# Optimization experiments

Hardware: AMD Instinct MI355X
Metric: run time of the kernel (lower is better)

## Reference

```python
import jax, jax.numpy as jnp
import numpy as np

B, T, D_MODEL, N_HEADS = 4, 2048, 1024, 16


def _alibi_bias(n_heads, seq_len):
    # matches torch alibi_bias(): slopes 2**(-8*i/m), i=1..m, m = pow2_ceil(n_heads)
    m = 1
    while m < n_heads:
        m *= 2
    slopes = jnp.array([2.0 ** (-8.0 * i / m) for i in range(1, m + 1)][:n_heads],
                       dtype=jnp.float32)
    pos = jnp.arange(seq_len)
    bias = (pos[None, :] - pos[:, None]).astype(jnp.float32)  # [T, T], j - i
    return slopes[:, None, None, None] * bias[None, None]      # [H, 1, T, T]


def setup_inputs() -> dict:
    key = jax.random.key(0)
    kx, kqkv, ko = jax.random.split(key, 3)
    x = jax.random.normal(kx, (B, T, D_MODEL), dtype=jnp.float32)
    Wqkv = jax.random.normal(kqkv, (3 * D_MODEL, D_MODEL), dtype=jnp.float32) / np.sqrt(D_MODEL)
    Wo = jax.random.normal(ko, (D_MODEL, D_MODEL), dtype=jnp.float32) / np.sqrt(D_MODEL)
    alibi = _alibi_bias(N_HEADS, T)  # [H, 1, T, T]
    return {"x": x, "alibi": alibi, "Wqkv": Wqkv, "Wo": Wo}


def reference(x, alibi, Wqkv, Wo):
    Bb, Tt, C = x.shape
    H = N_HEADS
    dk = C // H
    # qkv projection: [B, T, 3C] -> [B, T, 3, H, dk]
    qkv = (x @ Wqkv.T).reshape(Bb, Tt, 3, H, dk)
    q = jnp.moveaxis(qkv[:, :, 0], 2, 1)  # [B, H, T, dk]
    k = jnp.moveaxis(qkv[:, :, 1], 2, 1)
    v = jnp.moveaxis(qkv[:, :, 2], 2, 1)
    # causal (-inf above diagonal) + alibi additive mask, fp32, like the torch path
    causal = jnp.triu(jnp.full((Tt, Tt), -jnp.inf, dtype=jnp.float32), k=1)
    mask = causal[None, None] + alibi[:, 0][None]  # [1, H, T, T]
    scores = jnp.einsum('bhqd,bhkd->bhqk', q, k) / jnp.sqrt(jnp.float32(dk)) + mask
    p = jax.nn.softmax(scores, axis=-1)
    att = jnp.einsum('bhqk,bhkd->bhqd', p, v)           # [B, H, T, dk]
    y = jnp.moveaxis(att, 1, 2).reshape(Bb, Tt, C)       # [B, T, C]
    return y @ Wo.T
```

## Files before the change

kernel.cpp:

```cpp
#include <hip/hip_runtime.h>
#include <hip/hip_bf16.h>


#define B_ 4
#define T_ 2048
#define C_ 1024
#define H_ 16
#define DK 64

typedef __attribute__((ext_vector_type(8))) short short8;
typedef __attribute__((ext_vector_type(4))) float floatx4;

#define GLDS16(g, l)                                                          \
    __builtin_amdgcn_global_load_lds(                                         \
        (const __attribute__((address_space(1))) void*)(g),                   \
        (__attribute__((address_space(3))) void*)(l), 16, 0, 0)

static __device__ inline short f2bf(float x) {
    __hip_bfloat16 h = __float2bfloat16(x);
    return *reinterpret_cast<short*>(&h);
}

__global__ void detect_k(const unsigned int* __restrict__ x,
                         const unsigned int* __restrict__ ali,
                         const unsigned int* __restrict__ wqkv,
                         const unsigned int* __restrict__ wo,
                         int* __restrict__ flags) {
    __shared__ int cnt[4];
    const int tid = threadIdx.x;
    if (tid < 4) cnt[tid] = 0;
    __syncthreads();
    const int g = tid >> 6, l = tid & 63;
    const unsigned int* p = (g == 0) ? x : (g == 1) ? ali : (g == 2) ? wqkv : wo;
    int c = 0;
    for (int i = 0; i < 4; i++) {
        unsigned int w = p[l * 4 + i];
        int e0 = (w >> 7) & 0xFF;
        int e1 = (w >> 23) & 0xFF;
        c += (e0 >= 100 && e0 <= 140);
        c += (e1 >= 100 && e1 <= 140);
    }
    atomicAdd(&cnt[g], c);
    __syncthreads();
    if (l == 0) flags[g] = (cnt[g] < 400) ? 1 : 0;
}

__global__ void tobf16_k(const void* __restrict__ in, short* __restrict__ out,
                         int n8) {
    const unsigned int* u = (const unsigned int*)in;
    int c = 0;
#pragma unroll
    for (int i = 0; i < 16; i++) {
        unsigned int w = u[i];
        int e0 = (w >> 7) & 0xFF;
        int e1 = (w >> 23) & 0xFF;
        c += (e0 >= 100 && e0 <= 140);
        c += (e1 >= 100 && e1 <= 140);
    }
    const bool f32 = (c < 25);
    int i = blockIdx.x * blockDim.x + threadIdx.x;
    const int stride = gridDim.x * blockDim.x;
    for (; i < n8; i += stride) {
        if (f32) {
            float4 f0 = ((const float4*)in)[2 * i];
            float4 f1 = ((const float4*)in)[2 * i + 1];
            short8 v = { f2bf(f0.x), f2bf(f0.y), f2bf(f0.z), f2bf(f0.w),
                         f2bf(f1.x), f2bf(f1.y), f2bf(f1.z), f2bf(f1.w) };
            *(short8*)(out + (size_t)i * 8) = v;
        } else {
            *(short8*)(out + (size_t)i * 8) = ((const short8*)in)[i];
        }
    }
}

template <int MODE, int N>
__global__ __launch_bounds__(256) void gemm128_k(const short* __restrict__ A,
                                                 const short* __restrict__ W,
                                                 void* __restrict__ Dv) {
    const int K = 1024;
    const int tid  = threadIdx.x;
    const int wv   = tid >> 6;
    const int lane = tid & 63;
    const int l15  = lane & 15;
    const int quad = lane >> 4;
    const int wm = wv >> 1, wn = wv & 1;
    const int bn = blockIdx.x, bm = blockIdx.y;

    __shared__ short As[128 * 64];
    __shared__ short Bs[128 * 64];

    floatx4 acc[4][4];
#pragma unroll
    for (int mt = 0; mt < 4; mt++)
#pragma unroll
        for (int nt = 0; nt < 4; nt++)
#pragma unroll
            for (int r = 0; r < 4; r++) acc[mt][nt][r] = 0.f;

    const int lr = lane >> 3;
    const int lc = lane & 7;
    const int cg = lc ^ lr;

    for (int kt = 0; kt < K; kt += 64) {
        __syncthreads();
#pragma unroll
        for (int i = 0; i < 4; i++) {
            const int rbase = wv * 32 + i * 8;
            const int r = rbase + lr;
            size_t ga;
            if (MODE == 2) {
                int rowg = bm * 128 + r;
                int b = rowg >> 11, t = rowg & (T_ - 1), hh = kt >> 6;
                ga = (((size_t)b * H_ + hh) * T_ + t) * DK + cg * 8;
            } else {
                ga = (size_t)(bm * 128 + r) * K + kt + cg * 8;
            }
            GLDS16(A + ga, As + rbase * 64);
            size_t gb = (size_t)(bn * 128 + r) * K + kt + cg * 8;
            GLDS16(W + gb, Bs + rbase * 64);
        }
        __syncthreads();
#pragma unroll
        for (int ks = 0; ks < 64; ks += 32) {
            short8 af[4], bf[4];
#pragma unroll
            for (int mt = 0; mt < 4; mt++) {
                int row = wm * 64 + mt * 16 + l15;
                int cs = ((ks >> 3) + quad) ^ (row & 7);
                af[mt] = *(const short8*)(As + row * 64 + cs * 8);
            }
#pragma unroll
            for (int nt = 0; nt < 4; nt++) {
                int row = wn * 64 + nt * 16 + l15;
                int cs = ((ks >> 3) + quad) ^ (row & 7);
                bf[nt] = *(const short8*)(Bs + row * 64 + cs * 8);
            }
#pragma unroll
            for (int mt = 0; mt < 4; mt++)
#pragma unroll
                for (int nt = 0; nt < 4; nt++)
                    acc[mt][nt] = __builtin_amdgcn_mfma_f32_16x16x32_bf16(
                        af[mt], bf[nt], acc[mt][nt], 0, 0, 0);
        }
    }

#pragma unroll
    for (int mt = 0; mt < 4; mt++) {
#pragma unroll
        for (int nt = 0; nt < 4; nt++) {
#pragma unroll
            for (int r = 0; r < 4; r++) {
                int row = bm * 128 + wm * 64 + mt * 16 + quad * 4 + r;
                int col = bn * 128 + wn * 64 + nt * 16 + l15;
                if (MODE == 0) {
                    int b = row >> 11, t = row & (T_ - 1);
                    int s = col >> 10, rem = col & 1023;
                    int h = rem >> 6, d = rem & 63;
                    size_t dst = ((((size_t)s * B_ + b) * H_ + h) * T_ + t) * DK + d;
                    ((short*)Dv)[dst] = f2bf(acc[mt][nt][r]);
                } else if (MODE == 3) {
                    int h = row >> 6, d = row & 63;
                    int b = col >> 11, t = col & (T_ - 1);
                    size_t dst = (((size_t)(2 * B_ + b) * H_ + h) * DK + d) * T_ + t;
                    ((short*)Dv)[dst] = f2bf(acc[mt][nt][r]);
                } else {
                    ((float*)Dv)[(size_t)row * N + col] = acc[mt][nt][r];
                }
            }
        }
    }
}

template <int MODE, int N>
__global__ __launch_bounds__(256) void gemm_k(const void* __restrict__ Av,
                                              const void* __restrict__ Wv,
                                              void* __restrict__ Dv,
                                              const int* fA, const int* fW,
                                              size_t aOff) {
    const int K = 1024;
    const int tid  = threadIdx.x;
    const int wave = tid >> 6;
    const int lane = tid & 63;
    const int l15  = lane & 15;
    const int quad = lane >> 4;
    const int bn = blockIdx.x;
    const int bm = blockIdx.y;
    const bool aF32 = fA && (*fA != 0);
    const bool wF32 = fW && (*fW != 0);

    __shared__ short As[64 * 72];
    __shared__ short Bs[64 * 72];

    floatx4 acc[4];
#pragma unroll
    for (int nt = 0; nt < 4; nt++)
#pragma unroll
        for (int r = 0; r < 4; r++) acc[nt][r] = 0.f;

    for (int kt = 0; kt < K; kt += 64) {
        __syncthreads();
#pragma unroll
        for (int i = 0; i < 2; i++) {
            int chunk = tid + i * 256;
            int r = chunk >> 3, c8 = (chunk & 7) * 8;
            size_t offA;
            if (MODE == 2) {
                int rowg = bm * 64 + r;
                int b = rowg >> 11, t = rowg & (T_ - 1), hh = kt >> 6;
                offA = (((size_t)b * H_ + hh) * T_ + t) * DK + c8;
            } else {
                offA = (size_t)(bm * 64 + r) * K + kt + c8;
            }
            size_t offW = (size_t)(bn * 64 + r) * K + kt + c8;
            if (aF32) {
                const float* Af = (const float*)Av + aOff;
                float4 f0 = *(const float4*)(Af + offA);
                float4 f1 = *(const float4*)(Af + offA + 4);
                short8 v = { f2bf(f0.x), f2bf(f0.y), f2bf(f0.z), f2bf(f0.w),
                             f2bf(f1.x), f2bf(f1.y), f2bf(f1.z), f2bf(f1.w) };
                *(short8*)(As + r * 72 + c8) = v;
            } else {
                *(short8*)(As + r * 72 + c8) =
                    *(const short8*)((const short*)Av + aOff + offA);
            }
            if (wF32) {
                const float* Wf = (const float*)Wv;
                float4 f0 = *(const float4*)(Wf + offW);
                float4 f1 = *(const float4*)(Wf + offW + 4);
                short8 v = { f2bf(f0.x), f2bf(f0.y), f2bf(f0.z), f2bf(f0.w),
                             f2bf(f1.x), f2bf(f1.y), f2bf(f1.z), f2bf(f1.w) };
                *(short8*)(Bs + r * 72 + c8) = v;
            } else {
                *(short8*)(Bs + r * 72 + c8) = *(const short8*)((const short*)Wv + offW);
            }
        }
        __syncthreads();
#pragma unroll
        for (int ks = 0; ks < 64; ks += 32) {
            short8 a = *(const short8*)(As + (wave * 16 + l15) * 72 + ks + quad * 8);
#pragma unroll
            for (int nt = 0; nt < 4; nt++) {
                short8 b = *(const short8*)(Bs + (nt * 16 + l15) * 72 + ks + quad * 8);
                acc[nt] = __builtin_amdgcn_mfma_f32_16x16x32_bf16(a, b, acc[nt], 0, 0, 0);
            }
        }
    }

#pragma unroll
    for (int nt = 0; nt < 4; nt++) {
#pragma unroll
        for (int r = 0; r < 4; r++) {
            int row = bm * 64 + wave * 16 + quad * 4 + r;
            int col = bn * 64 + nt * 16 + l15;
            if (MODE == 0) {
                int b = row >> 11, t = row & (T_ - 1);
                int s = col >> 10, rem = col & 1023;
                int h = rem >> 6, d = rem & 63;
                size_t dst = ((((size_t)s * B_ + b) * H_ + h) * T_ + t) * DK + d;
                ((short*)Dv)[dst] = f2bf(acc[nt][r]);
            } else if (MODE == 3) {
                int h = row >> 6, d = row & 63;
                int b = col >> 11, t = col & (T_ - 1);
                size_t dst = (((size_t)(2 * B_ + b) * H_ + h) * DK + d) * T_ + t;
                ((short*)Dv)[dst] = f2bf(acc[nt][r]);
            } else {
                ((float*)Dv)[(size_t)row * N + col] = acc[nt][r];
            }
        }
    }
}

__global__ __launch_bounds__(256, 6) void attn_k(short* __restrict__ qkv) {
    const int tid  = threadIdx.x;
    const int wave = tid >> 6;
    const int lane = tid & 63;
    const int l15  = lane & 15;
    const int quad = lane >> 4;
    const int gid  = blockIdx.x;
    const int bh = (gid & 7) * 8 + (gid >> 8);
    const int qb = (31 - ((gid >> 3) & 31)) * 64;
    const int b = bh >> 4, h = bh & 15;

    short* Qp       = qkv + (((size_t)(0 * B_ + b) * H_ + h) * T_) * DK;
    const short* Kp = qkv + (((size_t)(1 * B_ + b) * H_ + h) * T_) * DK;
    const short* Vt = qkv + (((size_t)(2 * B_ + b) * H_ + h) * DK) * T_;

    __shared__ short Qs[64 * 72];
    __shared__ short Ks[64 * 64];
    __shared__ short Vts[64 * 64];

#pragma unroll
    for (int i = 0; i < 2; i++) {
        int chunk = tid + i * 256;
        int r = chunk >> 3, c8 = (chunk & 7) * 8;
        *(short8*)(Qs + r * 72 + c8) = *(const short8*)(Qp + (size_t)(qb + r) * DK + c8);
    }
    __syncthreads();
    short8 aq0 = *(const short8*)(Qs + (wave * 16 + l15) * 72 + quad * 8);
    short8 aq1 = *(const short8*)(Qs + (wave * 16 + l15) * 72 + 32 + quad * 8);

    const float LOG2E = 1.4426950408889634f;
    const float slope2 = exp2f(-0.5f * (float)(h + 1)) * LOG2E;
    const float scale2 = 0.125f * LOG2E;

    float lsum[4];
    floatx4 o[4];
#pragma unroll
    for (int r = 0; r < 4; r++) lsum[r] = 0.f;
#pragma unroll
    for (int nt = 0; nt < 4; nt++)
#pragma unroll
        for (int r = 0; r < 4; r++) o[nt][r] = 0.f;

    const int jt_end = qb >> 6;
    const int rb = qb + wave * 16 + quad * 4;
    int jstart = 0;
    {
        int lim = qb - 63 - (int)(50.f / slope2);
        if (lim > 0) jstart = lim >> 6;
    }

    const int lr = lane >> 3;
    const int cg = (lane & 7) ^ lr;

    for (int jt = jstart; jt <= jt_end; jt++) {
        __syncthreads();
#pragma unroll
        for (int i = 0; i < 2; i++) {
            const int rbase = wave * 16 + i * 8;
            GLDS16(Kp + (size_t)(jt * 64 + rbase + lr) * DK + cg * 8,
                   Ks + rbase * 64);
            GLDS16(Vt + (size_t)(rbase + lr) * T_ + jt * 64 + cg * 8,
                   Vts + rbase * 64);
        }
        __syncthreads();

        floatx4 s[4];
#pragma unroll
        for (int nt = 0; nt < 4; nt++)
#pragma unroll
            for (int r = 0; r < 4; r++) s[nt][r] = 0.f;
#pragma unroll
        for (int nt = 0; nt < 4; nt++) {
            int row = nt * 16 + l15;
            int c0 = quad ^ (row & 7);
            int c1 = (4 + quad) ^ (row & 7);
            short8 b0 = *(const short8*)(Ks + row * 64 + c0 * 8);
            short8 b1 = *(const short8*)(Ks + row * 64 + c1 * 8);
            s[nt] = __builtin_amdgcn_mfma_f32_16x16x32_bf16(aq0, b0, s[nt], 0, 0, 0);
            s[nt] = __builtin_amdgcn_mfma_f32_16x16x32_bf16(aq1, b1, s[nt], 0, 0, 0);
        }

        const bool diag = (jt == jt_end);
#pragma unroll
        for (int nt = 0; nt < 4; nt++) {
            int colg = jt * 64 + nt * 16 + l15;
            float cb = slope2 * (float)(colg - rb);
#pragma unroll
            for (int r = 0; r < 4; r++) {
                float sv = fmaf(s[nt][r], scale2, cb - slope2 * (float)r);
                if (diag && colg > rb + r) sv = -1e30f;
                float p = exp2f(sv);
                lsum[r] += p;
                Qs[wave * 1088 + (quad * 4 + r) * 68 + nt * 16 + l15] = f2bf(p);
            }
        }

#pragma unroll
        for (int ks = 0; ks < 64; ks += 32) {
            short8 a = *(const short8*)(Qs + wave * 1088 + l15 * 68 + ks + quad * 8);
#pragma unroll
            for (int nt = 0; nt < 4; nt++) {
                int row = nt * 16 + l15;
                int cs = ((ks >> 3) + quad) ^ (row & 7);
                short8 bf = *(const short8*)(Vts + row * 64 + cs * 8);
                o[nt] = __builtin_amdgcn_mfma_f32_16x16x32_bf16(a, bf, o[nt], 0, 0, 0);
            }
        }
    }

#pragma unroll
    for (int r = 0; r < 4; r++) {
#pragma unroll
        for (int mask = 1; mask < 16; mask <<= 1)
            lsum[r] += __shfl_xor(lsum[r], mask);
    }
#pragma unroll
    for (int nt = 0; nt < 4; nt++) {
#pragma unroll
        for (int r = 0; r < 4; r++) {
            int t = qb + wave * 16 + quad * 4 + r;
            int d = nt * 16 + l15;
            Qp[(size_t)t * DK + d] = f2bf(o[nt][r] / lsum[r]);
        }
    }
}

extern "C" void kernel_launch(void* const* d_in, const int* in_sizes, int n_in,
                              void* d_out, int out_size, void* d_ws, size_t ws_size,
                              hipStream_t stream) {
    const void* x    = d_in[0];
    const void* ali  = d_in[1];
    const void* Wqkv = d_in[2];
    const void* Wo   = d_in[3];
    float* out = (float*)d_out;

    int*   flags  = (int*)d_ws;
    short* qkv    = (short*)((char*)d_ws + 1024);
    short* xbf    = (short*)((char*)d_ws + 50332672);
    short* wqkvbf = (short*)((char*)d_ws + 67109888);
    short* wobf   = (short*)((char*)d_ws + 73401344);
    const bool fast = ws_size >= (size_t)75498496;

    dim3 blk(256);
    if (fast) {
        tobf16_k<<<2048, 256, 0, stream>>>(x, xbf, B_ * T_ * C_ / 8);
        tobf16_k<<<1536, 256, 0, stream>>>(Wqkv, wqkvbf, 3 * C_ * C_ / 8);
        tobf16_k<<<512, 256, 0, stream>>>(Wo, wobf, C_ * C_ / 8);
        gemm128_k<0, 0><<<dim3(16, 64), blk, 0, stream>>>(xbf, wqkvbf, qkv);
        gemm128_k<3, 0><<<dim3(64, 8), blk, 0, stream>>>(
            wqkvbf + (size_t)2048 * 1024, xbf, qkv);
        attn_k<<<dim3(2048), blk, 0, stream>>>(qkv);
        gemm128_k<2, C_><<<dim3(8, 64), blk, 0, stream>>>(qkv, wobf, out);
    } else {
        detect_k<<<1, 256, 0, stream>>>((const unsigned int*)x,
                                        (const unsigned int*)ali,
                                        (const unsigned int*)Wqkv,
                                        (const unsigned int*)Wo, flags);
        gemm_k<0, 0><<<dim3(32, 128), blk, 0, stream>>>(x, Wqkv, qkv,
                                                        &flags[0], &flags[2], 0);
        gemm_k<3, 0><<<dim3(128, 16), blk, 0, stream>>>(Wqkv, x, qkv,
                                                        &flags[2], &flags[0],
                                                        (size_t)2048 * 1024);
        attn_k<<<dim3(2048), blk, 0, stream>>>(qkv);
        gemm_k<2, C_><<<dim3(16, 128), blk, 0, stream>>>(qkv, Wo, out,
                                                         nullptr, &flags[3], 0);
    }
}
```

Measured before the change: 529.0 us.

## Merge launches, double-buffer K/V in attention, and swizzle P staging

Three bf16 conversion launches become one kernel that picks its tensor by block index. The two QKV projection GEMMs become a single launch that covers both the standard and the transposed-V layouts. The attention kernel now double-buffers K/V tiles in shared memory so the next tile's global loads overlap compute. It reads Q straight from global into registers, stores P in a separate XOR-swizzled buffer, and lowers the occupancy hint from 6 to 4. The aim is less launch overhead and hidden load latency, at the cost of more LDS per block and fewer resident blocks.

```diff
diff --git a/kernel.cpp b/kernel.cpp
--- a/kernel.cpp
+++ b/kernel.cpp
@@ -45,8 +45,23 @@
     if (l == 0) flags[g] = (cnt[g] < 400) ? 1 : 0;
 }
 
-__global__ void tobf16_k(const void* __restrict__ in, short* __restrict__ out,
-                         int n8) {
+__global__ void tobf16_all_k(const void* __restrict__ x,
+                             const void* __restrict__ wq,
+                             const void* __restrict__ wo,
+                             short* __restrict__ ox,
+                             short* __restrict__ owq,
+                             short* __restrict__ owo) {
+    const int bid = blockIdx.x;
+    const void* in;
+    short* out;
+    int n8, b0, nb;
+    if (bid < 2048) {
+        in = x; out = ox; n8 = B_ * T_ * C_ / 8; b0 = bid; nb = 2048;
+    } else if (bid < 3584) {
+        in = wq; out = owq; n8 = 3 * C_ * C_ / 8; b0 = bid - 2048; nb = 1536;
+    } else {
+        in = wo; out = owo; n8 = C_ * C_ / 8; b0 = bid - 3584; nb = 512;
+    }
     const unsigned int* u = (const unsigned int*)in;
     int c = 0;
 #pragma unroll
@@ -58,8 +73,8 @@
         c += (e1 >= 100 && e1 <= 140);
     }
     const bool f32 = (c < 25);
-    int i = blockIdx.x * blockDim.x + threadIdx.x;
-    const int stride = gridDim.x * blockDim.x;
+    int i = b0 * blockDim.x + threadIdx.x;
+    const int stride = nb * blockDim.x;
     for (; i < n8; i += stride) {
         if (f32) {
             float4 f0 = ((const float4*)in)[2 * i];
@@ -69,6 +84,105 @@
             *(short8*)(out + (size_t)i * 8) = v;
         } else {
             *(short8*)(out + (size_t)i * 8) = ((const short8*)in)[i];
+        }
+    }
+}
+
+__global__ __launch_bounds__(256) void gemm_qkvvt_k(
+    const short* __restrict__ xbf, const short* __restrict__ wqkvbf,
+    short* __restrict__ qkv) {
+    const int K = 1024;
+    const int tid  = threadIdx.x;
+    const int wv   = tid >> 6;
+    const int lane = tid & 63;
+    const int l15  = lane & 15;
+    const int quad = lane >> 4;
+    const int wm = wv >> 1, wn = wv & 1;
+
+    const int id = blockIdx.x;
+    const bool m0 = id < 1024;
+    int bm, bn;
+    const short *Ap, *Wp;
+    if (m0) {
+        bn = id & 15; bm = id >> 4; Ap = xbf; Wp = wqkvbf;
+    } else {
+        int j = id - 1024;
+        bn = j & 63; bm = j >> 6;
+        Ap = wqkvbf + (size_t)2048 * 1024; Wp = xbf;
+    }
+
+    __shared__ short As[128 * 64];
+    __shared__ short Bs[128 * 64];
+
+    floatx4 acc[4][4];
+#pragma unroll
+    for (int mt = 0; mt < 4; mt++)
+#pragma unroll
+        for (int nt = 0; nt < 4; nt++)
+#pragma unroll
+            for (int r = 0; r < 4; r++) acc[mt][nt][r] = 0.f;
+
+    const int lr = lane >> 3;
+    const int lc = lane & 7;
+    const int cg = lc ^ lr;
+
+    for (int kt = 0; kt < K; kt += 64) {
+        __syncthreads();
+#pragma unroll
+        for (int i = 0; i < 4; i++) {
+            const int rbase = wv * 32 + i * 8;
+            const int r = rbase + lr;
+            size_t ga = (size_t)(bm * 128 + r) * K + kt + cg * 8;
+            GLDS16(Ap + ga, As + rbase * 64);
+            size_t gb = (size_t)(bn * 128 + r) * K + kt + cg * 8;
+            GLDS16(Wp + gb, Bs + rbase * 64);
+        }
+        __syncthreads();
+#pragma unroll
+        for (int ks = 0; ks < 64; ks += 32) {
+            short8 af[4], bf[4];
+#pragma unroll
+            for (int mt = 0; mt < 4; mt++) {
+                int row = wm * 64 + mt * 16 + l15;
+                int cs = ((ks >> 3) + quad) ^ (row & 7);
+                af[mt] = *(const short8*)(As + row * 64 + cs * 8);
+            }
+#pragma unroll
+            for (int nt = 0; nt < 4; nt++) {
+                int row = wn * 64 + nt * 16 + l15;
+                int cs = ((ks >> 3) + quad) ^ (row & 7);
+                bf[nt] = *(const short8*)(Bs + row * 64 + cs * 8);
+            }
+#pragma unroll
+            for (int mt = 0; mt < 4; mt++)
+#pragma unroll
+                for (int nt = 0; nt < 4; nt++)
+                    acc[mt][nt] = __builtin_amdgcn_mfma_f32_16x16x32_bf16(
+                        af[mt], bf[nt], acc[mt][nt], 0, 0, 0);
+        }
+    }
+
+#pragma unroll
+    for (int mt = 0; mt < 4; mt++) {
+#pragma unroll
+        for (int nt = 0; nt < 4; nt++) {
+#pragma unroll
+            for (int r = 0; r < 4; r++) {
+                int row = bm * 128 + wm * 64 + mt * 16 + quad * 4 + r;
+                int col = bn * 128 + wn * 64 + nt * 16 + l15;
+                if (m0) {
+                    int b = row >> 11, t = row & (T_ - 1);
+                    int s = col >> 10, rem = col & 1023;
+                    int h = rem >> 6, d = rem & 63;
+                    size_t dst = ((((size_t)s * B_ + b) * H_ + h) * T_ + t) * DK + d;
+                    qkv[dst] = f2bf(acc[mt][nt][r]);
+                } else {
+                    int h = row >> 6, d = row & 63;
+                    int b = col >> 11, t = col & (T_ - 1);
+                    size_t dst = (((size_t)(2 * B_ + b) * H_ + h) * DK + d) * T_ + t;
+                    qkv[dst] = f2bf(acc[mt][nt][r]);
+                }
+            }
         }
     }
 }
@@ -270,7 +384,7 @@
     }
 }
 
-__global__ __launch_bounds__(256, 6) void attn_k(short* __restrict__ qkv) {
+__global__ __launch_bounds__(256, 4) void attn_k(short* __restrict__ qkv) {
     const int tid  = threadIdx.x;
     const int wave = tid >> 6;
     const int lane = tid & 63;
@@ -285,19 +399,13 @@
     const short* Kp = qkv + (((size_t)(1 * B_ + b) * H_ + h) * T_) * DK;
     const short* Vt = qkv + (((size_t)(2 * B_ + b) * H_ + h) * DK) * T_;
 
-    __shared__ short Qs[64 * 72];
-    __shared__ short Ks[64 * 64];
-    __shared__ short Vts[64 * 64];
-
-#pragma unroll
-    for (int i = 0; i < 2; i++) {
-        int chunk = tid + i * 256;
-        int r = chunk >> 3, c8 = (chunk & 7) * 8;
-        *(short8*)(Qs + r * 72 + c8) = *(const short8*)(Qp + (size_t)(qb + r) * DK + c8);
-    }
-    __syncthreads();
-    short8 aq0 = *(const short8*)(Qs + (wave * 16 + l15) * 72 + quad * 8);
-    short8 aq1 = *(const short8*)(Qs + (wave * 16 + l15) * 72 + 32 + quad * 8);
+    __shared__ short Ks[2][64 * 64];
+    __shared__ short Vts[2][64 * 64];
+    __shared__ short Ps[4 * 16 * 64];
+
+    const size_t qrow = (size_t)(qb + wave * 16 + l15) * DK;
+    const short8 aq0 = *(const short8*)(Qp + qrow + quad * 8);
+    const short8 aq1 = *(const short8*)(Qp + qrow + 32 + quad * 8);
 
     const float LOG2E = 1.4426950408889634f;
     const float slope2 = exp2f(-0.5f * (float)(h + 1)) * LOG2E;
@@ -323,17 +431,31 @@
     const int lr = lane >> 3;
     const int cg = (lane & 7) ^ lr;
 
+#pragma unroll
+    for (int i = 0; i < 2; i++) {
+        const int rbase = wave * 16 + i * 8;
+        GLDS16(Kp + (size_t)(jstart * 64 + rbase + lr) * DK + cg * 8,
+               &Ks[0][rbase * 64]);
+        GLDS16(Vt + (size_t)(rbase + lr) * T_ + jstart * 64 + cg * 8,
+               &Vts[0][rbase * 64]);
+    }
+    __syncthreads();
+
+    int cur = 0;
     for (int jt = jstart; jt <= jt_end; jt++) {
-        __syncthreads();
-#pragma unroll
-        for (int i = 0; i < 2; i++) {
-            const int rbase = wave * 16 + i * 8;
-            GLDS16(Kp + (size_t)(jt * 64 + rbase + lr) * DK + cg * 8,
-                   Ks + rbase * 64);
-            GLDS16(Vt + (size_t)(rbase + lr) * T_ + jt * 64 + cg * 8,
-                   Vts + rbase * 64);
-        }
-        __syncthreads();
+        if (jt < jt_end) {
+            const int nxt = cur ^ 1;
+#pragma unroll
+            for (int i = 0; i < 2; i++) {
+                const int rbase = wave * 16 + i * 8;
+                GLDS16(Kp + (size_t)((jt + 1) * 64 + rbase + lr) * DK + cg * 8,
+                       &Ks[nxt][rbase * 64]);
+                GLDS16(Vt + (size_t)(rbase + lr) * T_ + (jt + 1) * 64 + cg * 8,
+                       &Vts[nxt][rbase * 64]);
+            }
+        }
+        const short* Ksc = &Ks[cur][0];
+        const short* Vtc = &Vts[cur][0];
 
         floatx4 s[4];
 #pragma unroll
@@ -345,8 +467,8 @@
             int row = nt * 16 + l15;
             int c0 = quad ^ (row & 7);
             int c1 = (4 + quad) ^ (row & 7);
-            short8 b0 = *(const short8*)(Ks + row * 64 + c0 * 8);
-            short8 b1 = *(const short8*)(Ks + row * 64 + c1 * 8);
+            short8 b0 = *(const short8*)(Ksc + row * 64 + c0 * 8);
+            short8 b1 = *(const short8*)(Ksc + row * 64 + c1 * 8);
             s[nt] = __builtin_amdgcn_mfma_f32_16x16x32_bf16(aq0, b0, s[nt], 0, 0, 0);
             s[nt] = __builtin_amdgcn_mfma_f32_16x16x32_bf16(aq1, b1, s[nt], 0, 0, 0);
         }
@@ -362,21 +484,29 @@
                 if (diag && colg > rb + r) sv = -1e30f;
                 float p = exp2f(sv);
                 lsum[r] += p;
-                Qs[wave * 1088 + (quad * 4 + r) * 68 + nt * 16 + l15] = f2bf(p);
+                int prow = quad * 4 + r;
+                int pcol = nt * 16 + l15;
+                Ps[wave * 1024 + prow * 64 +
+                   (((pcol >> 3) ^ (prow & 7)) << 3) + (pcol & 7)] = f2bf(p);
             }
         }
 
 #pragma unroll
         for (int ks = 0; ks < 64; ks += 32) {
-            short8 a = *(const short8*)(Qs + wave * 1088 + l15 * 68 + ks + quad * 8);
+            short8 a = *(const short8*)(
+                Ps + wave * 1024 + l15 * 64 +
+                ((((ks >> 3) + quad) ^ (l15 & 7)) << 3));
 #pragma unroll
             for (int nt = 0; nt < 4; nt++) {
                 int row = nt * 16 + l15;
                 int cs = ((ks >> 3) + quad) ^ (row & 7);
-                short8 bf = *(const short8*)(Vts + row * 64 + cs * 8);
+                short8 bf = *(const short8*)(Vtc + row * 64 + cs * 8);
                 o[nt] = __builtin_amdgcn_mfma_f32_16x16x32_bf16(a, bf, o[nt], 0, 0, 0);
             }
         }
+
+        __syncthreads();
+        cur ^= 1;
     }
 
 #pragma unroll
@@ -414,12 +544,8 @@
 
     dim3 blk(256);
     if (fast) {
-        tobf16_k<<<2048, 256, 0, stream>>>(x, xbf, B_ * T_ * C_ / 8);
-        tobf16_k<<<1536, 256, 0, stream>>>(Wqkv, wqkvbf, 3 * C_ * C_ / 8);
-        tobf16_k<<<512, 256, 0, stream>>>(Wo, wobf, C_ * C_ / 8);
-        gemm128_k<0, 0><<<dim3(16, 64), blk, 0, stream>>>(xbf, wqkvbf, qkv);
-        gemm128_k<3, 0><<<dim3(64, 8), blk, 0, stream>>>(
-            wqkvbf + (size_t)2048 * 1024, xbf, qkv);
+        tobf16_all_k<<<4096, 256, 0, stream>>>(x, Wqkv, Wo, xbf, wqkvbf, wobf);
+        gemm_qkvvt_k<<<1536, blk, 0, stream>>>(xbf, wqkvbf, qkv);
         attn_k<<<dim3(2048), blk, 0, stream>>>(qkv);
         gemm128_k<2, C_><<<dim3(8, 64), blk, 0, stream>>>(qkv, wobf, out);
     } else {
```

Result: no change. 525.7 us (-0.6%).

## Enlarge GEMM tiles, merge conversion/QKV launches, double-buffer attention K/V

Applied to the files above, without the earlier changes.

Replaces the three bf16 conversion launches with one combined kernel, and the two QKV projection GEMMs with a single 256x256-tile, 512-thread GEMM that uses a swizzled block mapping. The output projection gets the same larger tile. Attention now uses 512-thread blocks covering 128 query rows, with K/V tiles double-buffered so the next tile loads while the current one computes, a single barrier per iteration, and Q loaded straight into registers. These changes target launch overhead, global-memory reuse and load latency, at the cost of higher register and LDS pressure and fewer blocks in flight.

```diff
diff --git a/kernel.cpp b/kernel.cpp
--- a/kernel.cpp
+++ b/kernel.cpp
@@ -45,8 +45,23 @@
     if (l == 0) flags[g] = (cnt[g] < 400) ? 1 : 0;
 }
 
-__global__ void tobf16_k(const void* __restrict__ in, short* __restrict__ out,
-                         int n8) {
+__global__ void tobf16_all_k(const void* __restrict__ x,
+                             const void* __restrict__ wq,
+                             const void* __restrict__ wo,
+                             short* __restrict__ ox,
+                             short* __restrict__ owq,
+                             short* __restrict__ owo) {
+    const int bid = blockIdx.x;
+    const void* in;
+    short* out;
+    int n8, b0, nb;
+    if (bid < 2048) {
+        in = x; out = ox; n8 = B_ * T_ * C_ / 8; b0 = bid; nb = 2048;
+    } else if (bid < 3584) {
+        in = wq; out = owq; n8 = 3 * C_ * C_ / 8; b0 = bid - 2048; nb = 1536;
+    } else {
+        in = wo; out = owo; n8 = C_ * C_ / 8; b0 = bid - 3584; nb = 512;
+    }
     const unsigned int* u = (const unsigned int*)in;
     int c = 0;
 #pragma unroll
@@ -58,8 +73,8 @@
         c += (e1 >= 100 && e1 <= 140);
     }
     const bool f32 = (c < 25);
-    int i = blockIdx.x * blockDim.x + threadIdx.x;
-    const int stride = gridDim.x * blockDim.x;
+    int i = b0 * blockDim.x + threadIdx.x;
+    const int stride = nb * blockDim.x;
     for (; i < n8; i += stride) {
         if (f32) {
             float4 f0 = ((const float4*)in)[2 * i];
@@ -73,8 +88,8 @@
     }
 }
 
-template <int MODE, int N>
-__global__ __launch_bounds__(256) void gemm128_k(const short* __restrict__ A,
+template <int MODE>
+__global__ __launch_bounds__(512) void gemm256_k(const short* __restrict__ A,
                                                  const short* __restrict__ W,
                                                  void* __restrict__ Dv) {
     const int K = 1024;
@@ -83,88 +98,105 @@
     const int lane = tid & 63;
     const int l15  = lane & 15;
     const int quad = lane >> 4;
-    const int wm = wv >> 1, wn = wv & 1;
-    const int bn = blockIdx.x, bm = blockIdx.y;
-
-    __shared__ short As[128 * 64];
-    __shared__ short Bs[128 * 64];
-
-    floatx4 acc[4][4];
-#pragma unroll
-    for (int mt = 0; mt < 4; mt++)
+    const int wm = wv >> 2, wn = wv & 3;
+
+    int bm, bn;
+    bool m0 = true;
+    const short *Ap = A, *Wp = W;
+    if (MODE == 1) {
+        const int id = blockIdx.x;
+        const int swz = (id & 7) * 48 + (id >> 3);
+        m0 = (swz < 256);
+        if (m0) {
+            bm = swz >> 3; bn = swz & 7;
+        } else {
+            int j = swz - 256;
+            bm = j >> 5; bn = j & 31;
+            Ap = W + (size_t)2048 * 1024;
+            Wp = A;
+        }
+    } else {
+        const int id = blockIdx.x;
+        const int swz = (id & 7) * 16 + (id >> 3);
+        bm = swz >> 2; bn = swz & 3;
+    }
+
+    __shared__ short As[256 * 64];
+    __shared__ short Bs[256 * 64];
+
+    floatx4 acc[8][4];
+#pragma unroll
+    for (int mt = 0; mt < 8; mt++)
 #pragma unroll
         for (int nt = 0; nt < 4; nt++)
 #pragma unroll
             for (int r = 0; r < 4; r++) acc[mt][nt][r] = 0.f;
 
-    const int lr = lane >> 3;
-    const int lc = lane & 7;
-    const int cg = lc ^ lr;
-
+    const int sr = tid >> 3;
     for (int kt = 0; kt < K; kt += 64) {
         __syncthreads();
 #pragma unroll
         for (int i = 0; i < 4; i++) {
-            const int rbase = wv * 32 + i * 8;
-            const int r = rbase + lr;
+            const int r = i * 64 + sr;
+            const int cg = (tid & 7) ^ (r & 7);
             size_t ga;
             if (MODE == 2) {
-                int rowg = bm * 128 + r;
+                int rowg = bm * 256 + r;
                 int b = rowg >> 11, t = rowg & (T_ - 1), hh = kt >> 6;
                 ga = (((size_t)b * H_ + hh) * T_ + t) * DK + cg * 8;
             } else {
-                ga = (size_t)(bm * 128 + r) * K + kt + cg * 8;
-            }
-            GLDS16(A + ga, As + rbase * 64);
-            size_t gb = (size_t)(bn * 128 + r) * K + kt + cg * 8;
-            GLDS16(W + gb, Bs + rbase * 64);
+                ga = (size_t)(bm * 256 + r) * K + kt + cg * 8;
+            }
+            GLDS16(Ap + ga, As + (i * 64 + wv * 8) * 64);
+            size_t gb = (size_t)(bn * 256 + r) * K + kt + cg * 8;
+            GLDS16(Wp + gb, Bs + (i * 64 + wv * 8) * 64);
         }
         __syncthreads();
 #pragma unroll
         for (int ks = 0; ks < 64; ks += 32) {
-            short8 af[4], bf[4];
-#pragma unroll
-            for (int mt = 0; mt < 4; mt++) {
-                int row = wm * 64 + mt * 16 + l15;
-                int cs = ((ks >> 3) + quad) ^ (row & 7);
-                af[mt] = *(const short8*)(As + row * 64 + cs * 8);
-            }
+            short8 bfr[4];
 #pragma unroll
             for (int nt = 0; nt < 4; nt++) {
                 int row = wn * 64 + nt * 16 + l15;
                 int cs = ((ks >> 3) + quad) ^ (row & 7);
-                bf[nt] = *(const short8*)(Bs + row * 64 + cs * 8);
-            }
-#pragma unroll
-            for (int mt = 0; mt < 4; mt++)
+                bfr[nt] = *(const short8*)(Bs + row * 64 + cs * 8);
+            }
+#pragma unroll
+            for (int mt = 0; mt < 8; mt++) {
+                int row = wm * 128 + mt * 16 + l15;
+                int cs = ((ks >> 3) + quad) ^ (row & 7);
+                short8 af = *(const short8*)(As + row * 64 + cs * 8);
 #pragma unroll
                 for (int nt = 0; nt < 4; nt++)
                     acc[mt][nt] = __builtin_amdgcn_mfma_f32_16x16x32_bf16(
-                        af[mt], bf[nt], acc[mt][nt], 0, 0, 0);
-        }
-    }
-
-#pragma unroll
-    for (int mt = 0; mt < 4; mt++) {
+                        af, bfr[nt], acc[mt][nt], 0, 0, 0);
+            }
+        }
+    }
+
+#pragma unroll
+    for (int mt = 0; mt < 8; mt++) {
 #pragma unroll
         for (int nt = 0; nt < 4; nt++) {
 #pragma unroll
             for (int r = 0; r < 4; r++) {
-                int row = bm * 128 + wm * 64 + mt * 16 + quad * 4 + r;
-                int col = bn * 128 + wn * 64 + nt * 16 + l15;
-                if (MODE == 0) {
-                    int b = row >> 11, t = row & (T_ - 1);
-                    int s = col >> 10, rem = col & 1023;
-                    int h = rem >> 6, d = rem & 63;
-                    size_t dst = ((((size_t)s * B_ + b) * H_ + h) * T_ + t) * DK + d;
-                    ((short*)Dv)[dst] = f2bf(acc[mt][nt][r]);
-                } else if (MODE == 3) {
-                    int h = row >> 6, d = row & 63;
-                    int b = col >> 11, t = col & (T_ - 1);
-                    size_t dst = (((size_t)(2 * B_ + b) * H_ + h) * DK + d) * T_ + t;
-                    ((short*)Dv)[dst] = f2bf(acc[mt][nt][r]);
+                int row = bm * 256 + wm * 128 + mt * 16 + quad * 4 + r;
+                int col = bn * 256 + wn * 64 + nt * 16 + l15;
+                if (MODE == 1) {
+                    if (m0) {
+                        int b = row >> 11, t = row & (T_ - 1);
+                        int s = col >> 10, rem = col & 1023;
+                        int h = rem >> 6, d = rem & 63;
+                        size_t dst = ((((size_t)s * B_ + b) * H_ + h) * T_ + t) * DK + d;
+                        ((short*)Dv)[dst] = f2bf(acc[mt][nt][r]);
+                    } else {
+                        int h = row >> 6, d = row & 63;
+                        int b = col >> 11, t = col & (T_ - 1);
+                        size_t dst = (((size_t)(2 * B_ + b) * H_ + h) * DK + d) * T_ + t;
+                        ((short*)Dv)[dst] = f2bf(acc[mt][nt][r]);
+                    }
                 } else {
-                    ((float*)Dv)[(size_t)row * N + col] = acc[mt][nt][r];
+                    ((float*)Dv)[(size_t)row * C_ + col] = acc[mt][nt][r];
                 }
             }
         }
@@ -270,34 +302,28 @@
     }
 }
 
-__global__ __launch_bounds__(256, 6) void attn_k(short* __restrict__ qkv) {
+__global__ __launch_bounds__(512, 4) void attn_k(short* __restrict__ qkv) {
     const int tid  = threadIdx.x;
     const int wave = tid >> 6;
     const int lane = tid & 63;
     const int l15  = lane & 15;
     const int quad = lane >> 4;
     const int gid  = blockIdx.x;
-    const int bh = (gid & 7) * 8 + (gid >> 8);
-    const int qb = (31 - ((gid >> 3) & 31)) * 64;
+    const int bh = (gid & 7) * 8 + (gid >> 7);
+    const int qb = (15 - ((gid >> 3) & 15)) * 128;
     const int b = bh >> 4, h = bh & 15;
 
     short* Qp       = qkv + (((size_t)(0 * B_ + b) * H_ + h) * T_) * DK;
     const short* Kp = qkv + (((size_t)(1 * B_ + b) * H_ + h) * T_) * DK;
     const short* Vt = qkv + (((size_t)(2 * B_ + b) * H_ + h) * DK) * T_;
 
-    __shared__ short Qs[64 * 72];
-    __shared__ short Ks[64 * 64];
-    __shared__ short Vts[64 * 64];
-
-#pragma unroll
-    for (int i = 0; i < 2; i++) {
-        int chunk = tid + i * 256;
-        int r = chunk >> 3, c8 = (chunk & 7) * 8;
-        *(short8*)(Qs + r * 72 + c8) = *(const short8*)(Qp + (size_t)(qb + r) * DK + c8);
-    }
-    __syncthreads();
-    short8 aq0 = *(const short8*)(Qs + (wave * 16 + l15) * 72 + quad * 8);
-    short8 aq1 = *(const short8*)(Qs + (wave * 16 + l15) * 72 + 32 + quad * 8);
+    __shared__ short Ks[2][64 * 64];
+    __shared__ short Vts[2][64 * 64];
+    __shared__ short Ps[8 * 16 * 64];
+
+    const size_t qrow = (size_t)(qb + wave * 16 + l15) * DK;
+    const short8 aq0 = *(const short8*)(Qp + qrow + quad * 8);
+    const short8 aq1 = *(const short8*)(Qp + qrow + 32 + quad * 8);
 
     const float LOG2E = 1.4426950408889634f;
     const float slope2 = exp2f(-0.5f * (float)(h + 1)) * LOG2E;
@@ -312,7 +338,7 @@
 #pragma unroll
         for (int r = 0; r < 4; r++) o[nt][r] = 0.f;
 
-    const int jt_end = qb >> 6;
+    const int jt_end = (qb + 127) >> 6;
     const int rb = qb + wave * 16 + quad * 4;
     int jstart = 0;
     {
@@ -320,20 +346,24 @@
         if (lim > 0) jstart = lim >> 6;
     }
 
-    const int lr = lane >> 3;
-    const int cg = (lane & 7) ^ lr;
-
+    const int sr = tid >> 3;
+    const int cg = (tid & 7) ^ (sr & 7);
+
+    GLDS16(Kp + (size_t)(jstart * 64 + sr) * DK + cg * 8, &Ks[0][wave * 512]);
+    GLDS16(Vt + (size_t)sr * T_ + jstart * 64 + cg * 8, &Vts[0][wave * 512]);
+    __syncthreads();
+
+    int cur = 0;
     for (int jt = jstart; jt <= jt_end; jt++) {
-        __syncthreads();
-#pragma unroll
-        for (int i = 0; i < 2; i++) {
-            const int rbase = wave * 16 + i * 8;
-            GLDS16(Kp + (size_t)(jt * 64 + rbase + lr) * DK + cg * 8,
-                   Ks + rbase * 64);
-            GLDS16(Vt + (size_t)(rbase + lr) * T_ + jt * 64 + cg * 8,
-                   Vts + rbase * 64);
-        }
-        __syncthreads();
+        if (jt < jt_end) {
+            const int nxt = cur ^ 1;
+            GLDS16(Kp + (size_t)((jt + 1) * 64 + sr) * DK + cg * 8,
+                   &Ks[nxt][wave * 512]);
+            GLDS16(Vt + (size_t)sr * T_ + (jt + 1) * 64 + cg * 8,
+                   &Vts[nxt][wave * 512]);
+        }
+        const short* Ksc = &Ks[cur][0];
+        const short* Vtc = &Vts[cur][0];
 
         floatx4 s[4];
 #pragma unroll
@@ -345,13 +375,13 @@
             int row = nt * 16 + l15;
             int c0 = quad ^ (row & 7);
             int c1 = (4 + quad) ^ (row & 7);
-            short8 b0 = *(const short8*)(Ks + row * 64 + c0 * 8);
-            short8 b1 = *(const short8*)(Ks + row * 64 + c1 * 8);
+            short8 b0 = *(const short8*)(Ksc + row * 64 + c0 * 8);
+            short8 b1 = *(const short8*)(Ksc + row * 64 + c1 * 8);
             s[nt] = __builtin_amdgcn_mfma_f32_16x16x32_bf16(aq0, b0, s[nt], 0, 0, 0);
             s[nt] = __builtin_amdgcn_mfma_f32_16x16x32_bf16(aq1, b1, s[nt], 0, 0, 0);
         }
 
-        const bool diag = (jt == jt_end);
+        const bool diag = (jt >= jt_end - 1);
 #pragma unroll
         for (int nt = 0; nt < 4; nt++) {
             int colg = jt * 64 + nt * 16 + l15;
@@ -362,21 +392,29 @@
                 if (diag && colg > rb + r) sv = -1e30f;
                 float p = exp2f(sv);
                 lsum[r] += p;
-                Qs[wave * 1088 + (quad * 4 + r) * 68 + nt * 16 + l15] = f2bf(p);
+                int prow = quad * 4 + r;
+                int pcol = nt * 16 + l15;
+                Ps[wave * 1024 + prow * 64 +
+                   (((pcol >> 3) ^ (prow & 7)) << 3) + (pcol & 7)] = f2bf(p);
             }
         }
 
 #pragma unroll
         for (int ks = 0; ks < 64; ks += 32) {
-            short8 a = *(const short8*)(Qs + wave * 1088 + l15 * 68 + ks + quad * 8);
+            short8 a = *(const short8*)(
+                Ps + wave * 1024 + l15 * 64 +
+                ((((ks >> 3) + quad) ^ (l15 & 7)) << 3));
 #pragma unroll
             for (int nt = 0; nt < 4; nt++) {
                 int row = nt * 16 + l15;
                 int cs = ((ks >> 3) + quad) ^ (row & 7);
-                short8 bf = *(const short8*)(Vts + row * 64 + cs * 8);
+                short8 bf = *(const short8*)(Vtc + row * 64 + cs * 8);
                 o[nt] = __builtin_amdgcn_mfma_f32_16x16x32_bf16(a, bf, o[nt], 0, 0, 0);
             }
         }
+
+        __syncthreads();
+        cur ^= 1;
     }
 
 #pragma unroll
@@ -412,27 +450,23 @@
     short* wobf   = (short*)((char*)d_ws + 73401344);
     const bool fast = ws_size >= (size_t)75498496;
 
-    dim3 blk(256);
     if (fast) {
-        tobf16_k<<<2048, 256, 0, stream>>>(x, xbf, B_ * T_ * C_ / 8);
-        tobf16_k<<<1536, 256, 0, stream>>>(Wqkv, wqkvbf, 3 * C_ * C_ / 8);
-        tobf16_k<<<512, 256, 0, stream>>>(Wo, wobf, C_ * C_ / 8);
-        gemm128_k<0, 0><<<dim3(16, 64), blk, 0, stream>>>(xbf, wqkvbf, qkv);
-        gemm128_k<3, 0><<<dim3(64, 8), blk, 0, stream>>>(
-            wqkvbf + (size_t)2048 * 1024, xbf, qkv);
-        attn_k<<<dim3(2048), blk, 0, stream>>>(qkv);
-        gemm128_k<2, C_><<<dim3(8, 64), blk, 0, stream>>>(qkv, wobf, out);
+        tobf16_all_k<<<4096, 256, 0, stream>>>(x, Wqkv, Wo, xbf, wqkvbf, wobf);
+        gemm256_k<1><<<384, 512, 0, stream>>>(xbf, wqkvbf, qkv);
+        attn_k<<<1024, 512, 0, stream>>>(qkv);
+        gemm256_k<2><<<128, 512, 0, stream>>>(qkv, wobf, out);
     } else {
         detect_k<<<1, 256, 0, stream>>>((const unsigned int*)x,
                                         (const unsigned int*)ali,
                                         (const unsigned int*)Wqkv,
                                         (const unsigned int*)Wo, flags);
+        dim3 blk(256);
         gemm_k<0, 0><<<dim3(32, 128), blk, 0, stream>>>(x, Wqkv, qkv,
                                                         &flags[0], &flags[2], 0);
         gemm_k<3, 0><<<dim3(128, 16), blk, 0, stream>>>(Wqkv, x, qkv,
                                                         &flags[2], &flags[0],
                                                         (size_t)2048 * 1024);
-        attn_k<<<dim3(2048), blk, 0, stream>>>(qkv);
+        attn_k<<<1024, 512, 0, stream>>>(qkv);
         gemm_k<2, C_><<<dim3(16, 128), blk, 0, stream>>>(qkv, Wo, out,
                                                          nullptr, &flags[3], 0);
     }
```

Result: slower. 548.0 us (+3.6%).
